# Optimization experiments

Measured on AMD Instinct MI355X. Metric: run time of the kernel, lower is better.

The kernel has to match this reference:

```python
import jax, jax.numpy as jnp
import numpy as np

B, T, C = 4, 2048, 1024
H, HS = 16, 64  # num_heads, head_size


def _rope_tables(seq_len, d):
    # RoFormer table: i = 1..d/2, theta_i = 1/10000^(2(i-1)/d)
    i = jnp.arange(1, d // 2 + 1, dtype=jnp.float32)
    thetas = 1.0 / (10000.0 ** (2.0 * (i - 1.0) / d))
    m_theta = jnp.arange(seq_len, dtype=jnp.float32)[:, None] * thetas  # [T, d/2]
    return jnp.sin(m_theta), jnp.cos(m_theta)


def _apply_rope(x, sin, cos):
    # x: [B, H, T, hs]; sin/cos: [T, hs/2] broadcast over B,H
    x1, x2 = x[..., 0::2], x[..., 1::2]
    return jnp.concatenate([x1 * cos - x2 * sin, x1 * sin + x2 * cos], axis=-1)


def setup_inputs() -> dict:
    key = jax.random.key(0)
    ks = jax.random.split(key, 5)
    s = 0.02
    return {
        "x": jax.random.normal(ks[0], (B, T, C), dtype=jnp.float32),
        "W_qkv": jax.random.normal(ks[1], (C, 3 * C), dtype=jnp.float32) * s,
        "b_qkv": jnp.zeros((3 * C,), dtype=jnp.float32),
        "W_o": jax.random.normal(ks[2], (C, C), dtype=jnp.float32) * s,
        "b_o": jnp.zeros((C,), dtype=jnp.float32),
    }


def reference(x, W_qkv, b_qkv, W_o, b_o):
    Bx, Tx, Cx = x.shape
    qkv = x @ W_qkv + b_qkv  # [B, T, 3C]
    q, k, v = jnp.split(qkv, 3, axis=-1)
    to_heads = lambda t: t.reshape(Bx, Tx, H, HS).transpose(0, 2, 1, 3)  # [B,H,T,hs]
    q, k, v = to_heads(q), to_heads(k), to_heads(v)

    sin, cos = _rope_tables(Tx, HS)
    q = _apply_rope(q, sin, cos)
    k = _apply_rope(k, sin, cos)

    scale = 1.0 / jnp.sqrt(jnp.asarray(HS, dtype=x.dtype))
    scores = jnp.einsum("bhqd,bhkd->bhqk", q, k) * scale
    causal = jnp.tril(jnp.ones((Tx, Tx), dtype=bool))
    scores = jnp.where(causal, scores, jnp.finfo(scores.dtype).min)
    attn = jax.nn.softmax(scores, axis=-1)
    out = jnp.einsum("bhqk,bhkd->bhqd", attn, v)  # [B,H,T,hs]
    out = out.transpose(0, 2, 1, 3).reshape(Bx, Tx, H * HS)
    return out @ W_o + b_o
```

## Files before the change

kernel.cpp:

```cpp
#include <hip/hip_runtime.h>
#include <math.h>

typedef float  f32x4 __attribute__((ext_vector_type(4)));
typedef float  f32x2 __attribute__((ext_vector_type(2)));
typedef __bf16 bf16x8 __attribute__((ext_vector_type(8)));
typedef unsigned short u16x8 __attribute__((ext_vector_type(8)));
typedef unsigned short u16x4 __attribute__((ext_vector_type(4)));

#define DEVI __device__ __forceinline__

constexpr int Bc = 4, Tc = 2048, Cc = 1024, Hc = 16, HSc = 64;
constexpr int Mc  = Bc * Tc;
constexpr int N1c = 3 * Cc;
constexpr int Kc  = Cc;

DEVI unsigned short f2bf(float f) {
    unsigned u = __builtin_bit_cast(unsigned, f);
    u += 0x7FFFu + ((u >> 16) & 1u);
    return (unsigned short)(u >> 16);
}
DEVI float bf2f(unsigned short s) {
    unsigned u = ((unsigned)s) << 16;
    return __builtin_bit_cast(float, u);
}

typedef const __attribute__((address_space(1))) void* gbl_vp;
typedef __attribute__((address_space(3))) void* lds_vp;
DEVI void gload16(const unsigned short* g, unsigned short* l) {
    __builtin_amdgcn_global_load_lds((gbl_vp)g, (lds_vp)l, 16, 0, 0);
}

__global__ void rope_tab_kernel(f32x2* __restrict__ tab)
{
    const int i = blockIdx.x * blockDim.x + threadIdx.x;
    const int t = i >> 5, d = i & 31;
    float theta = exp2f(-(float)d * 0.41524101186186f);
    float s, c;
    sincosf((float)t * theta, &s, &c);
    f32x2 v; v[0] = c; v[1] = s;
    tab[i] = v;
}

__global__ void cvt_kernel(const float* __restrict__ in,
                           unsigned short* __restrict__ out)
{
    const size_t i = ((size_t)blockIdx.x * blockDim.x + threadIdx.x) * 8;
    f32x4 a = *reinterpret_cast<const f32x4*>(in + i);
    f32x4 b = *reinterpret_cast<const f32x4*>(in + i + 4);
    u16x8 o;
    o[0] = f2bf(a[0]); o[1] = f2bf(a[1]); o[2] = f2bf(a[2]); o[3] = f2bf(a[3]);
    o[4] = f2bf(b[0]); o[5] = f2bf(b[1]); o[6] = f2bf(b[2]); o[7] = f2bf(b[3]);
    *reinterpret_cast<u16x8*>(out + i) = o;
}

__global__ void wt_kernel(const float* __restrict__ W,
                          unsigned short* __restrict__ Wt, int N, int K)
{
    __shared__ unsigned short Ts[64][72];
    const int tid = threadIdx.x;
    const int n0 = blockIdx.x * 64, k0 = blockIdx.y * 64;

    #pragma unroll
    for (int i = 0; i < 4; ++i) {
        int kr = (tid >> 4) + i * 16, nc = (tid & 15) * 4;
        f32x4 v = *reinterpret_cast<const f32x4*>(W + (size_t)(k0 + kr) * N + n0 + nc);
        #pragma unroll
        for (int e = 0; e < 4; ++e) Ts[kr][nc + e] = f2bf(v[e]);
    }
    __syncthreads();
    #pragma unroll
    for (int i = 0; i < 2; ++i) {
        int s = tid * 2 + i;
        int n = s >> 3, k8 = (s & 7) * 8;
        u16x8 o;
        #pragma unroll
        for (int j = 0; j < 8; ++j) o[j] = Ts[k8 + j][n];
        *reinterpret_cast<u16x8*>(Wt + (size_t)(n0 + n) * K + k0 + k8) = o;
    }
}

template <int MODE, int NCOLS>
__global__ void gemm_kernel(const unsigned short* __restrict__ A,
                            const unsigned short* __restrict__ Bt,
                            const float* __restrict__ bias,
                            const f32x2* __restrict__ rope_t,
                            unsigned short* __restrict__ q_out,
                            unsigned short* __restrict__ k_out,
                            unsigned short* __restrict__ v_out,
                            float* __restrict__ f_out)
{
    __shared__ unsigned short SM[2 * 128 * 64];
    unsigned short* As = SM;
    unsigned short* Bs = SM + 128 * 64;

    const int tid  = threadIdx.x;
    const int lane = tid & 63, wid = tid >> 6;
    const int wr = wid >> 1, wc = wid & 1;
    const int lrow = lane & 15, lk = lane >> 4;

    const int xcd = blockIdx.x & 7, loc = blockIdx.x >> 3;
    const int m0 = (xcd * 8 + (loc & 7)) * 128;
    const int n0 = (loc >> 3) * 128;

    f32x4 acc[4][4] = {};

    for (int kt = 0; kt < Kc / 64; ++kt) {
        const int k0 = kt * 64;
        #pragma unroll
        for (int i = 0; i < 4; ++i) {
            const int s   = ((i * 4 + wid) << 6) + lane;
            const int row = s >> 3;
            const int gc  = (s & 7) ^ (row & 7);
            gload16(A  + (size_t)(m0 + row) * Kc + k0 + gc * 8, &As[(i * 4 + wid) << 9]);
            gload16(Bt + (size_t)(n0 + row) * Kc + k0 + gc * 8, &Bs[(i * 4 + wid) << 9]);
        }
        __syncthreads();

        #pragma unroll
        for (int kk = 0; kk < 2; ++kk) {
            bf16x8 a[4], b[4];
            #pragma unroll
            for (int mt = 0; mt < 4; ++mt) {
                const int ra = wr * 64 + mt * 16 + lrow;
                a[mt] = __builtin_bit_cast(bf16x8,
                    *reinterpret_cast<const u16x8*>(&As[ra * 64 + (((kk * 4 + lk) ^ (ra & 7)) << 3)]));
            }
            #pragma unroll
            for (int nt = 0; nt < 4; ++nt) {
                const int rb = wc * 64 + nt * 16 + lrow;
                b[nt] = __builtin_bit_cast(bf16x8,
                    *reinterpret_cast<const u16x8*>(&Bs[rb * 64 + (((kk * 4 + lk) ^ (rb & 7)) << 3)]));
            }
            #pragma unroll
            for (int mt = 0; mt < 4; ++mt)
                #pragma unroll
                for (int nt = 0; nt < 4; ++nt)
                    acc[mt][nt] = __builtin_amdgcn_mfma_f32_16x16x32_bf16(a[mt], b[nt], acc[mt][nt], 0, 0, 0);
        }
        __syncthreads();
    }

    if constexpr (MODE == 1) {
        #pragma unroll
        for (int mt = 0; mt < 4; ++mt)
            #pragma unroll
            for (int nt = 0; nt < 4; ++nt)
                #pragma unroll
                for (int r = 0; r < 4; ++r) {
                    int grow = m0 + wr * 64 + mt * 16 + lk * 4 + r;
                    int gcol = n0 + wc * 64 + nt * 16 + lrow;
                    f_out[(size_t)grow * Cc + gcol] = acc[mt][nt][r] + bias[gcol];
                }
    } else if (n0 >= 2 * Cc) {
        unsigned short* Tv = SM;
        const int bb = m0 >> 11, t0 = m0 & (Tc - 1);
        #pragma unroll
        for (int p = 0; p < 2; ++p) {
            if (wc == p) {
                #pragma unroll
                for (int mt = 0; mt < 4; ++mt)
                    #pragma unroll
                    for (int nt = 0; nt < 4; ++nt)
                        #pragma unroll
                        for (int r = 0; r < 4; ++r) {
                            int hs_l = nt * 16 + lrow;
                            int t_l  = wr * 64 + mt * 16 + lk * 4 + r;
                            int gcol = n0 + wc * 64 + nt * 16 + lrow;
                            Tv[hs_l * 136 + t_l] = f2bf(acc[mt][nt][r] + bias[gcol]);
                        }
            }
            __syncthreads();
            const int h  = ((n0 - 2 * Cc) >> 6) + p;
            const int bh = bb * Hc + h;
            #pragma unroll
            for (int i = 0; i < 4; ++i) {
                int ch = i * 256 + tid;
                int hs = ch >> 4, tc = ch & 15;
                u16x8 v = *reinterpret_cast<const u16x8*>(&Tv[hs * 136 + tc * 8]);
                *reinterpret_cast<u16x8*>(
                    &v_out[((size_t)bh * HSc + hs) * Tc + t0 + tc * 8]) = v;
            }
            __syncthreads();
        }
    } else {
        unsigned short* dst = (n0 < Cc) ? q_out : k_out;
        #pragma unroll
        for (int mt = 0; mt < 4; ++mt)
            #pragma unroll
            for (int nt = 0; nt < 4; ++nt)
                #pragma unroll
                for (int r = 0; r < 4; ++r) {
                    int grow = m0 + wr * 64 + mt * 16 + lk * 4 + r;
                    int gcol = n0 + wc * 64 + nt * 16 + lrow;
                    float val = acc[mt][nt][r] + bias[gcol];
                    int cc   = gcol & (Cc - 1);
                    int h    = cc >> 6, hs = cc & 63;
                    int bb   = grow >> 11, t = grow & (Tc - 1);
                    int bh   = bb * Hc + h;
                    float partner = __shfl_xor(val, 1, 64);
                    const bool ev = !(lrow & 1);
                    float x1 = ev ? val : partner;
                    float x2 = ev ? partner : val;
                    int d = hs >> 1;
                    f32x2 cs = rope_t[t * 32 + d];
                    float o = ev ? (x1 * cs[0] - x2 * cs[1])
                                 : (x1 * cs[1] + x2 * cs[0]);
                    int hs_out = ev ? d : d + 32;
                    dst[((size_t)bh * Tc + t) * HSc + hs_out] = f2bf(o);
                }
    }
}

__launch_bounds__(256, 3)
__global__ void attn_kernel(const unsigned short* __restrict__ Q,
                            const unsigned short* __restrict__ K,
                            const unsigned short* __restrict__ Vt,
                            unsigned short* __restrict__ O)
{
    constexpr int PST = 72;
    __shared__ unsigned short Ks[2][64 * 64];
    __shared__ unsigned short Vs[2][64 * 64];
    __shared__ unsigned short Pl[4 * 32 * PST];

    const int tid = threadIdx.x, lane = tid & 63, wid = tid >> 6;
    const int lrow = lane & 15, lk = lane >> 4;

    const int xcd = blockIdx.x & 7, loc = blockIdx.x >> 3;
    const int bh  = xcd * 8 + (loc & 7);
    const int qs  = 15 - (loc >> 3);
    const int b = bh >> 4, h = bh & 15;

    const unsigned short* Qb = Q  + (size_t)bh * Tc  * HSc;
    const unsigned short* Kb = K  + (size_t)bh * Tc  * HSc;
    const unsigned short* Vb = Vt + (size_t)bh * HSc * Tc;
    unsigned short* pl = &Pl[wid * 32 * PST];

    auto stage = [&](int buf, int kt) {
        const int kv0 = kt * 64;
        #pragma unroll
        for (int rr = 0; rr < 2; ++rr) {
            const int s   = ((rr * 4 + wid) << 6) + lane;
            const int row = s >> 3;
            const int gc  = (s & 7) ^ (row & 7);
            gload16(Kb + (size_t)(kv0 + row) * HSc + gc * 8, &Ks[buf][(rr * 4 + wid) << 9]);
            gload16(Vb + (size_t)row * Tc + kv0 + gc * 8,    &Vs[buf][(rr * 4 + wid) << 9]);
        }
    };

    constexpr float sc = 0.18033688011112042f;

    const int wq0 = qs * 128 + wid * 32;
    const int ntile = 2 * qs + 2;

    bf16x8 qf[2][2];
    #pragma unroll
    for (int f = 0; f < 2; ++f)
        #pragma unroll
        for (int ks = 0; ks < 2; ++ks)
            qf[f][ks] = __builtin_bit_cast(bf16x8,
                *reinterpret_cast<const u16x8*>(Qb + (size_t)(wq0 + f * 16 + lrow) * HSc + ks * 32 + lk * 8));

    f32x4 Oacc[2][4] = {};
    float lsum[2][4] = {};

    stage(0, 0);
    for (int kt = 0; kt < ntile; ++kt) {
        const int kv0 = kt * 64;
        const int cur = kt & 1;
        const bool pre = (kt + 1 < ntile);
        if (pre) stage(cur ^ 1, kt + 1);
        if (pre) asm volatile("s_waitcnt vmcnt(4)" ::: "memory");
        else     asm volatile("s_waitcnt vmcnt(0)" ::: "memory");
        __builtin_amdgcn_s_barrier();

        if (kv0 <= wq0 + 31) {
            f32x4 S[2][4] = {};
            #pragma unroll
            for (int ct = 0; ct < 4; ++ct) {
                const int ro = ct * 16 + lrow;
                bf16x8 kf[2];
                #pragma unroll
                for (int ks = 0; ks < 2; ++ks)
                    kf[ks] = __builtin_bit_cast(bf16x8,
                        *reinterpret_cast<const u16x8*>(&Ks[cur][ro * 64 + (((ks * 4 + lk) ^ (ro & 7)) << 3)]));
                #pragma unroll
                for (int f = 0; f < 2; ++f)
                    #pragma unroll
                    for (int ks = 0; ks < 2; ++ks)
                        S[f][ct] = __builtin_amdgcn_mfma_f32_16x16x32_bf16(qf[f][ks], kf[ks], S[f][ct], 0, 0, 0);
            }

            #pragma unroll
            for (int f = 0; f < 2; ++f) {
                const bool mf = (kv0 + 63 > wq0 + f * 16);
                #pragma unroll
                for (int ct = 0; ct < 4; ++ct)
                    #pragma unroll
                    for (int r = 0; r < 4; ++r) {
                        float s = S[f][ct][r] * sc;
                        if (mf && (kv0 + ct * 16 + lrow > wq0 + f * 16 + lk * 4 + r)) s = -1e30f;
                        float pv = __builtin_amdgcn_exp2f(s);
                        lsum[f][r] += pv;
                        pl[(f * 16 + lk * 4 + r) * PST + ct * 16 + lrow] =
                            __builtin_bit_cast(unsigned short, (__bf16)pv);
                    }
            }
            asm volatile("s_waitcnt lgkmcnt(0)" ::: "memory");
            __builtin_amdgcn_sched_barrier(0);
            bf16x8 pf[2][2];
            #pragma unroll
            for (int f = 0; f < 2; ++f)
                #pragma unroll
                for (int ks = 0; ks < 2; ++ks)
                    pf[f][ks] = __builtin_bit_cast(bf16x8,
                        *reinterpret_cast<const u16x8*>(&pl[(f * 16 + lrow) * PST + ks * 32 + lk * 8]));

            #pragma unroll
            for (int nt = 0; nt < 4; ++nt) {
                const int ro = nt * 16 + lrow;
                bf16x8 vf[2];
                #pragma unroll
                for (int ks = 0; ks < 2; ++ks)
                    vf[ks] = __builtin_bit_cast(bf16x8,
                        *reinterpret_cast<const u16x8*>(&Vs[cur][ro * 64 + (((ks * 4 + lk) ^ (ro & 7)) << 3)]));
                #pragma unroll
                for (int f = 0; f < 2; ++f)
                    #pragma unroll
                    for (int ks = 0; ks < 2; ++ks)
                        Oacc[f][nt] = __builtin_amdgcn_mfma_f32_16x16x32_bf16(pf[f][ks], vf[ks], Oacc[f][nt], 0, 0, 0);
            }
        }
        asm volatile("s_waitcnt lgkmcnt(0)" ::: "memory");
        __builtin_amdgcn_sched_barrier(0);
        __builtin_amdgcn_s_barrier();
    }

    #pragma unroll
    for (int f = 0; f < 2; ++f) {
        #pragma unroll
        for (int mk = 1; mk < 16; mk <<= 1)
            #pragma unroll
            for (int r = 0; r < 4; ++r) lsum[f][r] += __shfl_xor(lsum[f][r], mk, 64);
        #pragma unroll
        for (int r = 0; r < 4; ++r) {
            float inv = 1.0f / lsum[f][r];
            int t = wq0 + f * 16 + lk * 4 + r;
            #pragma unroll
            for (int nt = 0; nt < 4; ++nt) {
                int col = h * 64 + nt * 16 + lrow;
                O[((size_t)b * Tc + t) * Cc + col] = f2bf(Oacc[f][nt][r] * inv);
            }
        }
    }
}

extern "C" void kernel_launch(void* const* d_in, const int* in_sizes, int n_in,
                              void* d_out, int out_size, void* d_ws, size_t ws_size,
                              hipStream_t stream)
{
    const float* x    = (const float*)d_in[0];
    const float* Wqkv = (const float*)d_in[1];
    const float* bqkv = (const float*)d_in[2];
    const float* Wo   = (const float*)d_in[3];
    const float* bo   = (const float*)d_in[4];
    float* out = (float*)d_out;

    char* ws = (char*)d_ws;
    size_t off = 0;
    auto alloc = [&](size_t bytes) {
        void* p = ws + off;
        off += (bytes + 255) & ~(size_t)255;
        return p;
    };
    const size_t elems = (size_t)Bc * Hc * Tc * HSc;
    unsigned short* Qb  = (unsigned short*)alloc(elems * 2);
    unsigned short* Kb  = (unsigned short*)alloc(elems * 2);
    unsigned short* Vt  = (unsigned short*)alloc(elems * 2);
    unsigned short* Oa  = (unsigned short*)alloc(elems * 2);
    unsigned short* Xb  = (unsigned short*)alloc((size_t)Mc * Kc * 2);
    unsigned short* Wq_t = (unsigned short*)alloc((size_t)N1c * Kc * 2);
    unsigned short* Wo_t = (unsigned short*)alloc((size_t)Cc * Kc * 2);
    f32x2* Rt = (f32x2*)alloc((size_t)Tc * 32 * 8);

    rope_tab_kernel<<<(Tc * 32) / 256, 256, 0, stream>>>(Rt);
    cvt_kernel<<<(Mc * Kc) / (256 * 8), 256, 0, stream>>>(x, Xb);
    wt_kernel<<<dim3(N1c / 64, Kc / 64), 256, 0, stream>>>(Wqkv, Wq_t, N1c, Kc);
    wt_kernel<<<dim3(Cc / 64, Kc / 64), 256, 0, stream>>>(Wo, Wo_t, Cc, Kc);

    gemm_kernel<0, N1c><<<(N1c / 128) * (Mc / 128), 256, 0, stream>>>(
        Xb, Wq_t, bqkv, Rt, Qb, Kb, Vt, nullptr);
    attn_kernel<<<1024, 256, 0, stream>>>(Qb, Kb, Vt, Oa);
    gemm_kernel<1, Cc><<<(Cc / 128) * (Mc / 128), 256, 0, stream>>>(
        Oa, Wo_t, bo, nullptr, nullptr, nullptr, nullptr, out);
}
```

Measured before the change: 184.3 us.

## Compute transposed scores and shuffle P to registers instead of LDS round-trip

The QK^T MFMA operands are swapped so each lane holds the scores of one query row across keys, which lets the softmax numerator be packed to bf16 and redistributed with cross-lane shuffles rather than written to and re-read from a per-wave LDS buffer. The softmax scale is folded into Q during the QKV projection epilogue, removing a multiply per score. Row sums become per-lane scalars reduced with fewer shuffles, and the launch bound is raised to four blocks per CU now that the P buffer is gone. This trades LDS traffic and waits for extra shuffle instructions and possibly more register pressure.

```diff
diff --git a/kernel.cpp b/kernel.cpp
--- a/kernel.cpp
+++ b/kernel.cpp
@@ -4,8 +4,9 @@
 typedef float  f32x4 __attribute__((ext_vector_type(4)));
 typedef float  f32x2 __attribute__((ext_vector_type(2)));
 typedef __bf16 bf16x8 __attribute__((ext_vector_type(8)));
+typedef __bf16 bf16x2 __attribute__((ext_vector_type(2)));
 typedef unsigned short u16x8 __attribute__((ext_vector_type(8)));
-typedef unsigned short u16x4 __attribute__((ext_vector_type(4)));
+typedef unsigned int   u32x4 __attribute__((ext_vector_type(4)));
 
 #define DEVI __device__ __forceinline__
 
@@ -18,10 +19,6 @@
     unsigned u = __builtin_bit_cast(unsigned, f);
     u += 0x7FFFu + ((u >> 16) & 1u);
     return (unsigned short)(u >> 16);
-}
-DEVI float bf2f(unsigned short s) {
-    unsigned u = ((unsigned)s) << 16;
-    return __builtin_bit_cast(float, u);
 }
 
 typedef const __attribute__((address_space(1))) void* gbl_vp;
@@ -183,7 +180,9 @@
             __syncthreads();
         }
     } else {
-        unsigned short* dst = (n0 < Cc) ? q_out : k_out;
+        const bool isQ = (n0 < Cc);
+        unsigned short* dst = isQ ? q_out : k_out;
+        const float oscale = isQ ? 0.18033688011112042f : 1.0f;
         #pragma unroll
         for (int mt = 0; mt < 4; ++mt)
             #pragma unroll
@@ -206,21 +205,19 @@
                     float o = ev ? (x1 * cs[0] - x2 * cs[1])
                                  : (x1 * cs[1] + x2 * cs[0]);
                     int hs_out = ev ? d : d + 32;
-                    dst[((size_t)bh * Tc + t) * HSc + hs_out] = f2bf(o);
+                    dst[((size_t)bh * Tc + t) * HSc + hs_out] = f2bf(o * oscale);
                 }
     }
 }
 
-__launch_bounds__(256, 3)
+__launch_bounds__(256, 4)
 __global__ void attn_kernel(const unsigned short* __restrict__ Q,
                             const unsigned short* __restrict__ K,
                             const unsigned short* __restrict__ Vt,
                             unsigned short* __restrict__ O)
 {
-    constexpr int PST = 72;
     __shared__ unsigned short Ks[2][64 * 64];
     __shared__ unsigned short Vs[2][64 * 64];
-    __shared__ unsigned short Pl[4 * 32 * PST];
 
     const int tid = threadIdx.x, lane = tid & 63, wid = tid >> 6;
     const int lrow = lane & 15, lk = lane >> 4;
@@ -233,7 +230,6 @@
     const unsigned short* Qb = Q  + (size_t)bh * Tc  * HSc;
     const unsigned short* Kb = K  + (size_t)bh * Tc  * HSc;
     const unsigned short* Vb = Vt + (size_t)bh * HSc * Tc;
-    unsigned short* pl = &Pl[wid * 32 * PST];
 
     auto stage = [&](int buf, int kt) {
         const int kv0 = kt * 64;
@@ -247,8 +243,6 @@
         }
     };
 
-    constexpr float sc = 0.18033688011112042f;
-
     const int wq0 = qs * 128 + wid * 32;
     const int ntile = 2 * qs + 2;
 
@@ -261,7 +255,10 @@
                 *reinterpret_cast<const u16x8*>(Qb + (size_t)(wq0 + f * 16 + lrow) * HSc + ks * 32 + lk * 8));
 
     f32x4 Oacc[2][4] = {};
-    float lsum[2][4] = {};
+    float lsum[2] = {0.f, 0.f};
+
+    const int sA = lrow + ((lane >> 4 & 1) << 5);
+    const int sB = sA + 16;
 
     stage(0, 0);
     for (int kt = 0; kt < ntile; ++kt) {
@@ -274,7 +271,7 @@
         __builtin_amdgcn_s_barrier();
 
         if (kv0 <= wq0 + 31) {
-            f32x4 S[2][4] = {};
+            unsigned pk[2][4][2];
             #pragma unroll
             for (int ct = 0; ct < 4; ++ct) {
                 const int ro = ct * 16 + lrow;
@@ -284,36 +281,48 @@
                     kf[ks] = __builtin_bit_cast(bf16x8,
                         *reinterpret_cast<const u16x8*>(&Ks[cur][ro * 64 + (((ks * 4 + lk) ^ (ro & 7)) << 3)]));
                 #pragma unroll
-                for (int f = 0; f < 2; ++f)
+                for (int f = 0; f < 2; ++f) {
+                    f32x4 S = {};
                     #pragma unroll
                     for (int ks = 0; ks < 2; ++ks)
-                        S[f][ct] = __builtin_amdgcn_mfma_f32_16x16x32_bf16(qf[f][ks], kf[ks], S[f][ct], 0, 0, 0);
-            }
-
-            #pragma unroll
-            for (int f = 0; f < 2; ++f) {
-                const bool mf = (kv0 + 63 > wq0 + f * 16);
-                #pragma unroll
-                for (int ct = 0; ct < 4; ++ct)
+                        S = __builtin_amdgcn_mfma_f32_16x16x32_bf16(kf[ks], qf[f][ks], S, 0, 0, 0);
+                    const bool mf = (kv0 + 63 > wq0 + f * 16);
+                    float pv[4];
                     #pragma unroll
                     for (int r = 0; r < 4; ++r) {
-                        float s = S[f][ct][r] * sc;
-                        if (mf && (kv0 + ct * 16 + lrow > wq0 + f * 16 + lk * 4 + r)) s = -1e30f;
-                        float pv = __builtin_amdgcn_exp2f(s);
-                        lsum[f][r] += pv;
-                        pl[(f * 16 + lk * 4 + r) * PST + ct * 16 + lrow] =
-                            __builtin_bit_cast(unsigned short, (__bf16)pv);
+                        float s = S[r];
+                        if (mf && (kv0 + ct * 16 + 4 * lk + r > wq0 + f * 16 + lrow)) s = -1e30f;
+                        pv[r] = __builtin_amdgcn_exp2f(s);
+                        lsum[f] += pv[r];
                     }
-            }
-            asm volatile("s_waitcnt lgkmcnt(0)" ::: "memory");
-            __builtin_amdgcn_sched_barrier(0);
+                    bf16x2 t0; t0[0] = (__bf16)pv[0]; t0[1] = (__bf16)pv[1];
+                    bf16x2 t1; t1[0] = (__bf16)pv[2]; t1[1] = (__bf16)pv[3];
+                    pk[f][ct][0] = __builtin_bit_cast(unsigned, t0);
+                    pk[f][ct][1] = __builtin_bit_cast(unsigned, t1);
+                }
+            }
+
+            const bool up = (lk >> 1);
             bf16x8 pf[2][2];
             #pragma unroll
             for (int f = 0; f < 2; ++f)
                 #pragma unroll
-                for (int ks = 0; ks < 2; ++ks)
-                    pf[f][ks] = __builtin_bit_cast(bf16x8,
-                        *reinterpret_cast<const u16x8*>(&pl[(f * 16 + lrow) * PST + ks * 32 + lk * 8]));
+                for (int ks = 0; ks < 2; ++ks) {
+                    u32x4 w;
+                    unsigned a0 = __shfl(pk[f][2 * ks][0],     sA, 64);
+                    unsigned b0 = __shfl(pk[f][2 * ks + 1][0], sA, 64);
+                    unsigned a1 = __shfl(pk[f][2 * ks][1],     sA, 64);
+                    unsigned b1 = __shfl(pk[f][2 * ks + 1][1], sA, 64);
+                    unsigned a2 = __shfl(pk[f][2 * ks][0],     sB, 64);
+                    unsigned b2 = __shfl(pk[f][2 * ks + 1][0], sB, 64);
+                    unsigned a3 = __shfl(pk[f][2 * ks][1],     sB, 64);
+                    unsigned b3 = __shfl(pk[f][2 * ks + 1][1], sB, 64);
+                    w[0] = up ? b0 : a0;
+                    w[1] = up ? b1 : a1;
+                    w[2] = up ? b2 : a2;
+                    w[3] = up ? b3 : a3;
+                    pf[f][ks] = __builtin_bit_cast(bf16x8, w);
+                }
 
             #pragma unroll
             for (int nt = 0; nt < 4; ++nt) {
@@ -337,13 +346,13 @@
 
     #pragma unroll
     for (int f = 0; f < 2; ++f) {
-        #pragma unroll
-        for (int mk = 1; mk < 16; mk <<= 1)
-            #pragma unroll
-            for (int r = 0; r < 4; ++r) lsum[f][r] += __shfl_xor(lsum[f][r], mk, 64);
+        float ls = lsum[f];
+        ls += __shfl_xor(ls, 16, 64);
+        ls += __shfl_xor(ls, 32, 64);
         #pragma unroll
         for (int r = 0; r < 4; ++r) {
-            float inv = 1.0f / lsum[f][r];
+            float lr = __shfl(ls, lk * 4 + r, 64);
+            float inv = 1.0f / lr;
             int t = wq0 + f * 16 + lk * 4 + r;
             #pragma unroll
             for (int nt = 0; nt < 4; ++nt) {
```

Result: no change. 185.7 us (+0.7%).
